# Performance work log

Hardware: AMD Instinct MI355X
Metric: run time of the kernel (lower is better)

## Reference

```python
import jax, jax.numpy as jnp
import numpy as np

D = 256
K = 64


def setup_inputs() -> dict:
    key = jax.random.key(0)
    k1, k2, k3 = jax.random.split(key, 3)
    B, H, W = 16, 96, 96
    X = jax.random.normal(k1, (B, D, H, W), dtype=jnp.float32)
    std1 = 1.0 / float(np.sqrt(K * D))
    std2 = 1.0 / float(np.sqrt(K))
    codewords = jax.random.uniform(k2, (K, D), dtype=jnp.float32, minval=-std1, maxval=std1)
    scale = jax.random.uniform(k3, (K,), dtype=jnp.float32, minval=-std2, maxval=std2)
    return {"X": X, "codewords": codewords, "scale": scale}


def reference(X, codewords, scale):
    # X: [B, D, H, W] -> Xf: [B, N, D]
    B = X.shape[0]
    Xf = X.reshape(B, X.shape[1], -1).transpose(0, 2, 1)
    # Scaled L2 distances: SL[b,n,k] = scale[k] * ||x_bn - c_k||^2
    x2 = jnp.sum(Xf * Xf, axis=-1, keepdims=True)          # [B, N, 1]
    c2 = jnp.sum(codewords * codewords, axis=-1)            # [K]
    xc = jnp.einsum('bnd,kd->bnk', Xf, codewords)           # [B, N, K]
    SL = scale * (x2 - 2.0 * xc + c2)                       # [B, N, K]
    # Assignment weights: softmax over codewords K
    A = jax.nn.softmax(SL, axis=-1)                         # [B, N, K]
    # Aggregate residuals: E[b,k,d] = sum_n A[b,n,k] * (X[b,n,d] - C[k,d])
    E = jnp.einsum('bnk,bnd->bkd', A, Xf) - jnp.sum(A, axis=1)[:, :, None] * codewords
    return E
```

## Files before the change

kernel.cpp:

```cpp
#include <hip/hip_runtime.h>

#define NDIM  256
#define NK    64
#define NPIX  9216
#define NB    16
#define TN    64
#define NW    32
#define GRID  (NB*NW)

typedef _Float16 half2_t __attribute__((ext_vector_type(2)));
typedef _Float16 half4_t __attribute__((ext_vector_type(4)));
typedef _Float16 half8_t __attribute__((ext_vector_type(8)));
typedef float    f32x4  __attribute__((ext_vector_type(4)));

__device__ __forceinline__ float fdot2(half2_t a, half2_t b, float c) {
  return __builtin_amdgcn_fdot2(a, b, c, false);
}

#define BAR() asm volatile("s_waitcnt lgkmcnt(0)\n\ts_barrier" ::: "memory")

#define OFF_ASUM   0
#define OFF_APART  (NB * NK)
#define OFF_EPART  (OFF_APART + GRID * NK)
#define WS_NEED    ((size_t)OFF_EPART * 4 + (size_t)GRID * NK * NDIM * 2)

__global__ __launch_bounds__(256, 2) void encode_main(
    const float* __restrict__ X, const float* __restrict__ Cw,
    const float* __restrict__ scale,
    void* __restrict__ Eout, float* __restrict__ Aout, int mode)
{
  __shared__ _Float16 XbS[32 * 66 * 8];
  __shared__ _Float16 Al[NK][72];
  __shared__ float red2[4][TN];
  __shared__ float redM[4][TN];
  __shared__ float redS[4][TN];

  const int tid  = threadIdx.x;
  const int w    = __builtin_amdgcn_readfirstlane(tid >> 6);
  const int lane = tid & 63;
  const int m    = lane & 15, quad = lane >> 4;
  const int b    = blockIdx.x >> 5;
  const int wid  = blockIdx.x & 31;
  const int ntiles = (wid < 16) ? 5 : 4;
  const int pix0   = (wid * 4 + (wid < 16 ? wid : 16)) * TN;
  const float* Xbase = X + (size_t)b * NDIM * NPIX;
  const int kbase = w * 16;

  float xv[64];
  {
    const float* Xg = Xbase + (size_t)(w * 64) * NPIX + pix0 + lane;
#pragma unroll
    for (int i = 0; i < 64; ++i) xv[i] = Xg[(size_t)i * NPIX];
  }

  {
    const int kk = tid >> 2, ch = tid & 3;
    const float* Cr = Cw + kk * NDIM + ch * 64;
    float s = 0.f;
#pragma unroll
    for (int j = 0; j < 16; ++j) {
      const float4 v = *(const float4*)(Cr + 4 * j);
      s += v.x * v.x + v.y * v.y + v.z * v.z + v.w * v.w;
    }
    redM[ch][kk] = s;
  }

  half8_t af1[8];
#pragma unroll
  for (int ks = 0; ks < 8; ++ks) {
    const float* ap = Cw + (kbase + m) * NDIM + ks * 32 + quad * 8;
    const float4 a0 = *(const float4*)(ap);
    const float4 a1 = *(const float4*)(ap + 4);
    half8_t h;
    h[0] = (_Float16)a0.x; h[1] = (_Float16)a0.y;
    h[2] = (_Float16)a0.z; h[3] = (_Float16)a0.w;
    h[4] = (_Float16)a1.x; h[5] = (_Float16)a1.y;
    h[6] = (_Float16)a1.z; h[7] = (_Float16)a1.w;
    af1[ks] = h;
  }

  const float4 scv = *(const float4*)(scale + kbase + quad * 4);
  const float sc[4] = {scv.x, scv.y, scv.z, scv.w};

  BAR();
  float sq[4];
#pragma unroll
  for (int r = 0; r < 4; ++r) {
    const int k = kbase + quad * 4 + r;
    const float c2k = redM[0][k] + redM[1][k] + redM[2][k] + redM[3][k];
    sq[r] = sc[r] * c2k;
  }

  f32x4 acc_e[4][4];
#pragma unroll
  for (int i = 0; i < 4; ++i)
#pragma unroll
    for (int j = 0; j < 4; ++j)
      acc_e[i][j] = (f32x4){0.f, 0.f, 0.f, 0.f};
  float asum_acc = 0.f;

  for (int tt = 0; tt < ntiles; ++tt) {
    BAR();

    {
      const bool more = (tt + 1 < ntiles);
      const float* Xgn = Xbase + (size_t)(w * 64) * NPIX + pix0 + (tt + 1) * TN + lane;
      float xsq = 0.f;
#pragma unroll
      for (int g = 0; g < 8; ++g) {
        half8_t hv;
#pragma unroll
        for (int i = 0; i < 8; ++i) {
          const float v = xv[g * 8 + i];
          hv[i] = (_Float16)v; xsq += v * v;
        }
        *(half8_t*)&XbS[((w * 8 + g) * 66 + lane) * 8] = hv;
        if (more) {
#pragma unroll
          for (int i = 0; i < 8; ++i)
            xv[g * 8 + i] = Xgn[(size_t)(g * 8 + i) * NPIX];
        }
      }
      red2[w][lane] = xsq;
    }
    BAR();

    f32x4 accs[4];
#pragma unroll
    for (int nt = 0; nt < 4; ++nt) accs[nt] = (f32x4){0.f, 0.f, 0.f, 0.f};
#pragma unroll
    for (int ks = 0; ks < 8; ++ks) {
#pragma unroll
      for (int nt = 0; nt < 4; ++nt) {
        const half8_t bf = *(const half8_t*)&XbS[((ks * 4 + quad) * 66 + nt * 16 + m) * 8];
        accs[nt] = __builtin_amdgcn_mfma_f32_16x16x32_f16(af1[ks], bf, accs[nt], 0, 0, 0);
      }
    }

    float e[4][4], mw[4];
#pragma unroll
    for (int nt = 0; nt < 4; ++nt) {
      const int p = nt * 16 + m;
      const float x2p = red2[0][p] + red2[1][p] + red2[2][p] + red2[3][p];
      float L[4];
      float mx = -3.0e38f;
#pragma unroll
      for (int r = 0; r < 4; ++r) {
        L[r] = sc[r] * x2p - 2.f * sc[r] * accs[nt][r] + sq[r];
        mx = fmaxf(mx, L[r]);
      }
      mx = fmaxf(mx, __shfl_xor(mx, 16));
      mx = fmaxf(mx, __shfl_xor(mx, 32));
      float s = 0.f;
#pragma unroll
      for (int r = 0; r < 4; ++r) { e[nt][r] = __expf(L[r] - mx); s += e[nt][r]; }
      s += __shfl_xor(s, 16);
      s += __shfl_xor(s, 32);
      mw[nt] = mx;
      if (lane < 16) { redM[w][p] = mx; redS[w][p] = s; }
    }
    BAR();
#pragma unroll
    for (int nt = 0; nt < 4; ++nt) {
      const int p = nt * 16 + m;
      const float M = fmaxf(fmaxf(redM[0][p], redM[1][p]),
                            fmaxf(redM[2][p], redM[3][p]));
      const float T = redS[0][p] * __expf(redM[0][p] - M)
                    + redS[1][p] * __expf(redM[1][p] - M)
                    + redS[2][p] * __expf(redM[2][p] - M)
                    + redS[3][p] * __expf(redM[3][p] - M);
      const float norm = __expf(mw[nt] - M) / T;
#pragma unroll
      for (int r = 0; r < 4; ++r)
        Al[kbase + quad * 4 + r][p] = (_Float16)(e[nt][r] * norm);
    }
    BAR();

#pragma unroll
    for (int ks = 0; ks < 2; ++ks) {
      half8_t ba[4];
#pragma unroll
      for (int kt = 0; kt < 4; ++kt)
        ba[kt] = *(const half8_t*)&Al[kt * 16 + m][ks * 32 + quad * 8];
#pragma unroll
      for (int dt = 0; dt < 4; ++dt) {
        const int c = w * 8 + dt * 2 + (m >> 3);
        const int dlow = m & 7;
        half8_t xa;
#pragma unroll
        for (int j = 0; j < 8; ++j)
          xa[j] = XbS[(c * 66 + ks * 32 + quad * 8 + j) * 8 + dlow];
#pragma unroll
        for (int kt = 0; kt < 4; ++kt)
          acc_e[dt][kt] = __builtin_amdgcn_mfma_f32_16x16x32_f16(xa, ba[kt], acc_e[dt][kt], 0, 0, 0);
      }
    }

    {
      const half2_t one = {(_Float16)1.f, (_Float16)1.f};
      const int ka = kbase + (lane >> 2);
      const int pa = (lane & 3) * 16;
      float s = 0.f;
#pragma unroll
      for (int lc = 0; lc < 2; ++lc) {
        const half8_t sv = *(const half8_t*)&Al[ka][pa + lc * 8];
        s = fdot2(__builtin_shufflevector(sv, sv, 0, 1), one, s);
        s = fdot2(__builtin_shufflevector(sv, sv, 2, 3), one, s);
        s = fdot2(__builtin_shufflevector(sv, sv, 4, 5), one, s);
        s = fdot2(__builtin_shufflevector(sv, sv, 6, 7), one, s);
      }
      s += __shfl_xor(s, 1);
      s += __shfl_xor(s, 2);
      asum_acc += s;
    }
  }

  BAR();
  _Float16* Et = XbS;
#pragma unroll
  for (int dt = 0; dt < 4; ++dt)
#pragma unroll
    for (int kt = 0; kt < 4; ++kt)
#pragma unroll
      for (int r = 0; r < 4; ++r) {
        const int k = kt * 16 + m;
        const int d = w * 64 + dt * 16 + quad * 4 + r;
        Et[k * 264 + d] = (_Float16)acc_e[dt][kt][r];
      }
  BAR();
  const int ko = tid >> 2, cq = tid & 3;
  if (mode) {
    _Float16* Ebk = (_Float16*)Eout + (size_t)blockIdx.x * (NK * NDIM);
#pragma unroll
    for (int g = 0; g < 8; ++g)
      *(half8_t*)&Ebk[ko * NDIM + cq * 64 + g * 8] =
          *(const half8_t*)&Et[ko * 264 + cq * 64 + g * 8];
    if ((lane & 3) == 0)
      Aout[blockIdx.x * NK + kbase + (lane >> 2)] = asum_acc;
  } else {
    float* Ebk = (float*)Eout + (size_t)b * (NK * NDIM);
#pragma unroll
    for (int g = 0; g < 64; ++g)
      atomicAdd(&Ebk[ko * NDIM + cq * 64 + g], (float)Et[ko * 264 + cq * 64 + g]);
    if ((lane & 3) == 0)
      atomicAdd(&Aout[b * NK + kbase + (lane >> 2)], asum_acc);
  }
}

__global__ void finalize_partials(const _Float16* __restrict__ EpartH,
                                  const float* __restrict__ Apart,
                                  const float* __restrict__ Cw,
                                  float* __restrict__ out) {
  const int g = blockIdx.x * 256 + threadIdx.x;
  const int i0 = g * 4;
  const int bb = i0 >> 14;
  const int o  = i0 & 16383;
  const int k  = o >> 8, d = i0 & 255;
  float a = 0.f;
#pragma unroll 8
  for (int w = 0; w < NW; ++w) a += Apart[(bb * NW + w) * NK + k];
  float s0 = 0.f, s1 = 0.f, s2 = 0.f, s3 = 0.f;
  const _Float16* base = EpartH + (((size_t)bb * NW) << 14) + o;
#pragma unroll 4
  for (int w = 0; w < NW; ++w) {
    const half4_t v = *(const half4_t*)(base + ((size_t)w << 14));
    s0 += (float)v[0]; s1 += (float)v[1];
    s2 += (float)v[2]; s3 += (float)v[3];
  }
  const float4 c0 = *(const float4*)(Cw + k * NDIM + d);
  float4 r0;
  r0.x = s0 - a * c0.x; r0.y = s1 - a * c0.y;
  r0.z = s2 - a * c0.z; r0.w = s3 - a * c0.w;
  *(float4*)(out + i0) = r0;
}

__global__ void finalize_atomic(const float* __restrict__ E_acc,
                                const float* __restrict__ asum,
                                const float* __restrict__ Cw,
                                float* __restrict__ out) {
  const int i = blockIdx.x * 256 + threadIdx.x;
  const int d = i & 255;
  const int k = (i >> 8) & 63;
  const int bb = i >> 14;
  out[i] = E_acc[i] - asum[bb * NK + k] * Cw[k * NDIM + d];
}

extern "C" void kernel_launch(void* const* d_in, const int* in_sizes, int n_in,
                              void* d_out, int out_size, void* d_ws, size_t ws_size,
                              hipStream_t stream) {
  const float* X     = (const float*)d_in[0];
  const float* Cw    = (const float*)d_in[1];
  const float* scale = (const float*)d_in[2];
  float* out = (float*)d_out;

  float* wsf = (float*)d_ws;
  float* asum  = wsf + OFF_ASUM;
  float* Apart = wsf + OFF_APART;

  if (ws_size >= WS_NEED) {
    _Float16* EpartH = (_Float16*)(wsf + OFF_EPART);
    encode_main<<<GRID, 256, 0, stream>>>(X, Cw, scale, EpartH, Apart, 1);
    finalize_partials<<<(NB*NK*NDIM)/(256*4), 256, 0, stream>>>(EpartH, Apart, Cw, out);
  } else {
    float* E_acc = wsf + OFF_APART;
    hipMemsetAsync(wsf, 0,
                   (size_t)(NB*NK + NB*NK*NDIM) * sizeof(float), stream);
    encode_main<<<GRID, 256, 0, stream>>>(X, Cw, scale, E_acc, asum, 0);
    finalize_atomic<<<(NB*NK*NDIM)/256, 256, 0, stream>>>(E_acc, asum, Cw, out);
  }
}
```

Measured before the change: 255.8 us.

## Double-buffer the X tile in LDS and raise wave priority around MFMA loops

The shared X tile becomes two buffers. Each iteration computes on the current buffer while the next tile is converted to fp16 and written into the other buffer after the compute phase. This drops one barrier per tile and moves the global prefetch of tile t+2 further ahead of its use. It also adds s_setprio around both MFMA loops and a sched_barrier in the codeword fp16 conversion loop. The cost is doubled LDS for X, which could limit how many blocks fit per CU, and longer register live ranges for the prefetched values.

```diff
diff --git a/kernel.cpp b/kernel.cpp
--- a/kernel.cpp
+++ b/kernel.cpp
@@ -29,7 +29,7 @@
     const float* __restrict__ scale,
     void* __restrict__ Eout, float* __restrict__ Aout, int mode)
 {
-  __shared__ _Float16 XbS[32 * 66 * 8];
+  __shared__ _Float16 XbS[2][32 * 66 * 8];
   __shared__ _Float16 Al[NK][72];
   __shared__ float red2[4][TN];
   __shared__ float redM[4][TN];
@@ -77,6 +77,7 @@
     h[4] = (_Float16)a1.x; h[5] = (_Float16)a1.y;
     h[6] = (_Float16)a1.z; h[7] = (_Float16)a1.w;
     af1[ks] = h;
+    __builtin_amdgcn_sched_barrier(0);
   }
 
   const float4 scv = *(const float4*)(scale + kbase + quad * 4);
@@ -99,43 +100,47 @@
       acc_e[i][j] = (f32x4){0.f, 0.f, 0.f, 0.f};
   float asum_acc = 0.f;
 
+  auto STAGE = [&](int bufi) {
+    _Float16* Xb = XbS[bufi];
+    float xsq = 0.f;
+#pragma unroll
+    for (int g = 0; g < 8; ++g) {
+      half8_t hv;
+#pragma unroll
+      for (int i = 0; i < 8; ++i) {
+        const float v = xv[g * 8 + i];
+        hv[i] = (_Float16)v; xsq += v * v;
+      }
+      *(half8_t*)&Xb[((w * 8 + g) * 66 + lane) * 8] = hv;
+    }
+    red2[w][lane] = xsq;
+  };
+  auto ISSUE = [&](int t) {
+    const float* Xg = Xbase + (size_t)(w * 64) * NPIX + pix0 + t * TN + lane;
+#pragma unroll
+    for (int i = 0; i < 64; ++i) xv[i] = Xg[(size_t)i * NPIX];
+  };
+
+  STAGE(0);
+  ISSUE(1);
+  BAR();
+
   for (int tt = 0; tt < ntiles; ++tt) {
-    BAR();
-
-    {
-      const bool more = (tt + 1 < ntiles);
-      const float* Xgn = Xbase + (size_t)(w * 64) * NPIX + pix0 + (tt + 1) * TN + lane;
-      float xsq = 0.f;
-#pragma unroll
-      for (int g = 0; g < 8; ++g) {
-        half8_t hv;
-#pragma unroll
-        for (int i = 0; i < 8; ++i) {
-          const float v = xv[g * 8 + i];
-          hv[i] = (_Float16)v; xsq += v * v;
-        }
-        *(half8_t*)&XbS[((w * 8 + g) * 66 + lane) * 8] = hv;
-        if (more) {
-#pragma unroll
-          for (int i = 0; i < 8; ++i)
-            xv[g * 8 + i] = Xgn[(size_t)(g * 8 + i) * NPIX];
-        }
-      }
-      red2[w][lane] = xsq;
-    }
-    BAR();
+    const _Float16* Xb = XbS[tt & 1];
 
     f32x4 accs[4];
 #pragma unroll
     for (int nt = 0; nt < 4; ++nt) accs[nt] = (f32x4){0.f, 0.f, 0.f, 0.f};
+    __builtin_amdgcn_s_setprio(1);
 #pragma unroll
     for (int ks = 0; ks < 8; ++ks) {
 #pragma unroll
       for (int nt = 0; nt < 4; ++nt) {
-        const half8_t bf = *(const half8_t*)&XbS[((ks * 4 + quad) * 66 + nt * 16 + m) * 8];
+        const half8_t bf = *(const half8_t*)&Xb[((ks * 4 + quad) * 66 + nt * 16 + m) * 8];
         accs[nt] = __builtin_amdgcn_mfma_f32_16x16x32_f16(af1[ks], bf, accs[nt], 0, 0, 0);
       }
     }
+    __builtin_amdgcn_s_setprio(0);
 
     float e[4][4], mw[4];
 #pragma unroll
@@ -176,6 +181,7 @@
     }
     BAR();
 
+    __builtin_amdgcn_s_setprio(1);
 #pragma unroll
     for (int ks = 0; ks < 2; ++ks) {
       half8_t ba[4];
@@ -189,12 +195,13 @@
         half8_t xa;
 #pragma unroll
         for (int j = 0; j < 8; ++j)
-          xa[j] = XbS[(c * 66 + ks * 32 + quad * 8 + j) * 8 + dlow];
+          xa[j] = Xb[(c * 66 + ks * 32 + quad * 8 + j) * 8 + dlow];
 #pragma unroll
         for (int kt = 0; kt < 4; ++kt)
           acc_e[dt][kt] = __builtin_amdgcn_mfma_f32_16x16x32_f16(xa, ba[kt], acc_e[dt][kt], 0, 0, 0);
       }
     }
+    __builtin_amdgcn_s_setprio(0);
 
     {
       const half2_t one = {(_Float16)1.f, (_Float16)1.f};
@@ -213,10 +220,16 @@
       s += __shfl_xor(s, 2);
       asum_acc += s;
     }
+
+    if (tt + 1 < ntiles) {
+      STAGE((tt + 1) & 1);
+      if (tt + 2 < ntiles) ISSUE(tt + 2);
+      BAR();
+    }
   }
 
   BAR();
-  _Float16* Et = XbS;
+  _Float16* Et = XbS[0];
 #pragma unroll
   for (int dt = 0; dt < 4; ++dt)
 #pragma unroll
```

Measured after the change: 239.3 us. 1.07x faster.

## Rebalance grid to 48 blocks per batch with 3 tiles and occupancy 3

Applied to the files above, without the earlier changes.

Splits each batch over 48 blocks of three 64-pixel tiles each, replacing the uneven 4/5-tile split. Launch bounds rise to 3 blocks per SIMD group. The shared X buffer gets a padded slot layout meant to cut LDS bank conflicts. The next-tile X prefetch moves after the barrier as one 64-load batch, and s_setprio raises wave priority around the MFMA sections. Higher occupancy limits registers, which risks spills given the 64-float prefetch array and the accumulators. More blocks also mean more partial results to reduce.

```diff
diff --git a/kernel.cpp b/kernel.cpp
--- a/kernel.cpp
+++ b/kernel.cpp
@@ -5,7 +5,8 @@
 #define NPIX  9216
 #define NB    16
 #define TN    64
-#define NW    32
+#define NW    48
+#define TPB   3
 #define GRID  (NB*NW)
 
 typedef _Float16 half2_t __attribute__((ext_vector_type(2)));
@@ -17,6 +18,8 @@
   return __builtin_amdgcn_fdot2(a, b, c, false);
 }
 
+#define SLOT(g, p) ((g) * 72 + (p) + ((p) >> 3))
+
 #define BAR() asm volatile("s_waitcnt lgkmcnt(0)\n\ts_barrier" ::: "memory")
 
 #define OFF_ASUM   0
@@ -24,12 +27,12 @@
 #define OFF_EPART  (OFF_APART + GRID * NK)
 #define WS_NEED    ((size_t)OFF_EPART * 4 + (size_t)GRID * NK * NDIM * 2)
 
-__global__ __launch_bounds__(256, 2) void encode_main(
+__global__ __launch_bounds__(256, 3) void encode_main(
     const float* __restrict__ X, const float* __restrict__ Cw,
     const float* __restrict__ scale,
     void* __restrict__ Eout, float* __restrict__ Aout, int mode)
 {
-  __shared__ _Float16 XbS[32 * 66 * 8];
+  __shared__ _Float16 XbS[32 * 72 * 8];
   __shared__ _Float16 Al[NK][72];
   __shared__ float red2[4][TN];
   __shared__ float redM[4][TN];
@@ -39,10 +42,9 @@
   const int w    = __builtin_amdgcn_readfirstlane(tid >> 6);
   const int lane = tid & 63;
   const int m    = lane & 15, quad = lane >> 4;
-  const int b    = blockIdx.x >> 5;
-  const int wid  = blockIdx.x & 31;
-  const int ntiles = (wid < 16) ? 5 : 4;
-  const int pix0   = (wid * 4 + (wid < 16 ? wid : 16)) * TN;
+  const int b    = blockIdx.x / NW;
+  const int wid  = blockIdx.x % NW;
+  const int pix0 = wid * (TPB * TN);
   const float* Xbase = X + (size_t)b * NDIM * NPIX;
   const int kbase = w * 16;
 
@@ -77,6 +79,7 @@
     h[4] = (_Float16)a1.x; h[5] = (_Float16)a1.y;
     h[6] = (_Float16)a1.z; h[7] = (_Float16)a1.w;
     af1[ks] = h;
+    __builtin_amdgcn_sched_barrier(0);
   }
 
   const float4 scv = *(const float4*)(scale + kbase + quad * 4);
@@ -99,12 +102,10 @@
       acc_e[i][j] = (f32x4){0.f, 0.f, 0.f, 0.f};
   float asum_acc = 0.f;
 
-  for (int tt = 0; tt < ntiles; ++tt) {
+  for (int tt = 0; tt < TPB; ++tt) {
     BAR();
 
     {
-      const bool more = (tt + 1 < ntiles);
-      const float* Xgn = Xbase + (size_t)(w * 64) * NPIX + pix0 + (tt + 1) * TN + lane;
       float xsq = 0.f;
 #pragma unroll
       for (int g = 0; g < 8; ++g) {
@@ -114,28 +115,31 @@
           const float v = xv[g * 8 + i];
           hv[i] = (_Float16)v; xsq += v * v;
         }
-        *(half8_t*)&XbS[((w * 8 + g) * 66 + lane) * 8] = hv;
-        if (more) {
-#pragma unroll
-          for (int i = 0; i < 8; ++i)
-            xv[g * 8 + i] = Xgn[(size_t)(g * 8 + i) * NPIX];
-        }
+        *(half8_t*)&XbS[SLOT(w * 8 + g, lane) * 8] = hv;
       }
       red2[w][lane] = xsq;
     }
     BAR();
 
+    if (tt + 1 < TPB) {
+      const float* Xg = Xbase + (size_t)(w * 64) * NPIX + pix0 + (tt + 1) * TN + lane;
+#pragma unroll
+      for (int i = 0; i < 64; ++i) xv[i] = Xg[(size_t)i * NPIX];
+    }
+
     f32x4 accs[4];
 #pragma unroll
     for (int nt = 0; nt < 4; ++nt) accs[nt] = (f32x4){0.f, 0.f, 0.f, 0.f};
+    __builtin_amdgcn_s_setprio(1);
 #pragma unroll
     for (int ks = 0; ks < 8; ++ks) {
 #pragma unroll
       for (int nt = 0; nt < 4; ++nt) {
-        const half8_t bf = *(const half8_t*)&XbS[((ks * 4 + quad) * 66 + nt * 16 + m) * 8];
+        const half8_t bf = *(const half8_t*)&XbS[SLOT(ks * 4 + quad, nt * 16 + m) * 8];
         accs[nt] = __builtin_amdgcn_mfma_f32_16x16x32_f16(af1[ks], bf, accs[nt], 0, 0, 0);
       }
     }
+    __builtin_amdgcn_s_setprio(0);
 
     float e[4][4], mw[4];
 #pragma unroll
@@ -176,6 +180,7 @@
     }
     BAR();
 
+    __builtin_amdgcn_s_setprio(1);
 #pragma unroll
     for (int ks = 0; ks < 2; ++ks) {
       half8_t ba[4];
@@ -189,12 +194,13 @@
         half8_t xa;
 #pragma unroll
         for (int j = 0; j < 8; ++j)
-          xa[j] = XbS[(c * 66 + ks * 32 + quad * 8 + j) * 8 + dlow];
+          xa[j] = XbS[SLOT(c, ks * 32 + quad * 8 + j) * 8 + dlow];
 #pragma unroll
         for (int kt = 0; kt < 4; ++kt)
           acc_e[dt][kt] = __builtin_amdgcn_mfma_f32_16x16x32_f16(xa, ba[kt], acc_e[dt][kt], 0, 0, 0);
       }
     }
+    __builtin_amdgcn_s_setprio(0);
 
     {
       const half2_t one = {(_Float16)1.f, (_Float16)1.f};
```

Measured after the change: 369.1 us. 1.44x slower.
